# Kernel optimization log

Hardware: AMD Instinct MI355X
Metric: run time of the kernel (lower is better)

## Reference

```python
import jax, jax.numpy as jnp
import numpy as np

NUM_EXPERTS = 16
TOP_K = 2


def _swiglu(x, w13, w2):
    # x: [t, d]; w13: [2I, d] (gate and up fused); w2: [d, I]
    h = x @ w13.T                      # [t, 2I]
    gate, up = jnp.split(h, 2, axis=-1)
    return (jax.nn.silu(gate) * up) @ w2.T  # [t, d]


def setup_inputs() -> dict:
    key = jax.random.key(0)
    ks = jax.random.split(key, 6)
    T, D, I, E, SI = 4096, 1024, 512, NUM_EXPERTS, 2048
    return {
        "hidden_states": jax.random.normal(ks[0], (T, D), jnp.float32),
        "router_logits": jax.random.normal(ks[1], (T, E), jnp.float32),
        "w13": jax.random.normal(ks[2], (E, 2 * I, D), jnp.float32) * (1.0 / np.sqrt(D)),
        "w2": jax.random.normal(ks[3], (E, D, I), jnp.float32) * (1.0 / np.sqrt(I)),
        "w13_shared": jax.random.normal(ks[4], (2 * SI, D), jnp.float32) * (1.0 / np.sqrt(D)),
        "w2_shared": jax.random.normal(ks[5], (D, SI), jnp.float32) * (1.0 / np.sqrt(SI)),
    }


def reference(hidden_states, router_logits, w13, w2, w13_shared, w2_shared):
    # Shared expert path (overlapped with routed dispatch in the original).
    shared_out = _swiglu(hidden_states, w13_shared, w2_shared)  # [T, d]

    # Routing: softmax -> top-k -> renormalize (vLLM FusedMoE w/ renormalize=True).
    probs = jax.nn.softmax(router_logits, axis=-1)              # [T, E]
    topk_w, topk_idx = jax.lax.top_k(probs, TOP_K)              # [T, k]
    topk_w = topk_w / jnp.sum(topk_w, axis=-1, keepdims=True)

    # Dense combine-weight matrix [T, E]: zero where expert not selected.
    T = hidden_states.shape[0]
    combine = jnp.zeros((T, NUM_EXPERTS), hidden_states.dtype)
    combine = combine.at[jnp.arange(T)[:, None], topk_idx].add(topk_w)

    # Grouped expert compute: scan over experts (fixed structural set),
    # accumulating the combine-weighted SwiGLU output. Memory-friendly: no
    # [E, T, 2I] intermediate is materialized.
    def body(acc, ew):
        w13_e, w2_e, c_e = ew                     # [2I,d], [d,I], [T]
        y = _swiglu(hidden_states, w13_e, w2_e)   # [T, d]
        return acc + c_e[:, None] * y, None

    fused_out, _ = jax.lax.scan(body, jnp.zeros_like(hidden_states),
                                (w13, w2, combine.T))
    return shared_out, fused_out
```

## Files before the change

### kernel.cpp

```cpp
#include <hip/hip_runtime.h>


#define T_TOK 4096
#define NEXP  16

typedef __attribute__((ext_vector_type(8))) short   short8;
typedef __attribute__((ext_vector_type(4))) float   floatx4;

typedef __attribute__((address_space(1))) void as1_void;
typedef __attribute__((address_space(3))) void as3_void;

__device__ __forceinline__ float bf2f(ushort u) {
    union { unsigned int i; float f; } v; v.i = ((unsigned int)u) << 16; return v.f;
}
__device__ __forceinline__ ushort f2bf(float f) {
    unsigned int u = __builtin_bit_cast(unsigned int, f);
    unsigned int r = 0x7FFFu + ((u >> 16) & 1u);
    return (ushort)((u + r) >> 16);
}

__device__ __forceinline__ float load_elem(const void* p, long i, int bf) {
    return bf ? bf2f(((const ushort*)p)[i]) : ((const float*)p)[i];
}

__global__ void detect_dtype(const ushort* __restrict__ xu, int* __restrict__ dflag) {
    __shared__ int cnt;
    if (threadIdx.x == 0) cnt = 0;
    __syncthreads();
    int ok = 0;
    for (int i = threadIdx.x; i < 512; i += 256) {
        int e = (xu[2 * i] >> 7) & 0xFF;
        ok += (e >= 90 && e <= 140) ? 1 : 0;
    }
    atomicAdd(&cnt, ok);
    __syncthreads();
    if (threadIdx.x == 0) *dflag = (cnt >= 384) ? 1 : 0;
}

__global__ void detect_xsel(const void* __restrict__ p0, const void* __restrict__ p4,
                            const int* __restrict__ dflag, int* __restrict__ xsel) {
    __shared__ float s0s, s4s;
    if (threadIdx.x == 0) { s0s = 0.f; s4s = 0.f; }
    __syncthreads();
    int bf = *dflag;
    float a0 = 0.f, a4 = 0.f;
    for (int i = threadIdx.x; i < 4096; i += 256) {
        a0 += fabsf(load_elem(p0, (long)i * 997 + 13, bf));
        a4 += fabsf(load_elem(p4, (long)i * 997 + 13, bf));
    }
    atomicAdd(&s0s, a0);
    atomicAdd(&s4s, a4);
    __syncthreads();
    if (threadIdx.x == 0) *xsel = (s0s >= s4s) ? 0 : 1;
}

__device__ __forceinline__ void top2(const void* logits, int t, int bf,
                                     int& b0, int& b1, float& w0, float& w1) {
    float l[16];
#pragma unroll
    for (int j = 0; j < 16; ++j) l[j] = load_elem(logits, t * 16 + j, bf);
    b0 = 0; float v0 = l[0];
#pragma unroll
    for (int j = 1; j < 16; ++j) { if (l[j] > v0) { v0 = l[j]; b0 = j; } }
    b1 = -1; float v1 = -3.4e38f;
#pragma unroll
    for (int j = 0; j < 16; ++j) {
        if (j == b0) continue;
        if (l[j] > v1) { v1 = l[j]; b1 = j; }
    }
    float d = __expf(v1 - v0);
    w0 = 1.0f / (1.0f + d);
    w1 = d / (1.0f + d);
}

__global__ void router_counts(const void* __restrict__ logits, const int* __restrict__ dflag,
                              int* __restrict__ counts) {
    int t = blockIdx.x * blockDim.x + threadIdx.x;
    if (t >= T_TOK) return;
    int b0, b1; float w0, w1;
    top2(logits, t, *dflag, b0, b1, w0, w1);
    atomicAdd(&counts[b0], 1);
    atomicAdd(&counts[b1], 1);
}

__global__ void scan_kernel(const int* __restrict__ counts, int* __restrict__ offsets) {
    if (threadIdx.x == 0 && blockIdx.x == 0) {
        int acc = 0;
        for (int e = 0; e < NEXP; ++e) { offsets[e] = acc; acc += counts[e]; }
    }
}

__global__ void router_pairs(const void* __restrict__ logits, const int* __restrict__ dflag,
                             const int* __restrict__ offsets, int* __restrict__ cursor,
                             int* __restrict__ pairinfo, float* __restrict__ pairw) {
    int t = blockIdx.x * blockDim.x + threadIdx.x;
    if (t >= T_TOK) return;
    int b0, b1; float w0, w1;
    top2(logits, t, *dflag, b0, b1, w0, w1);
    int p0 = offsets[b0] + atomicAdd(&cursor[b0], 1);
    pairinfo[p0] = 2 * t;     pairw[p0] = w0;
    int p1 = offsets[b1] + atomicAdd(&cursor[b1], 1);
    pairinfo[p1] = 2 * t + 1; pairw[p1] = w1;
}

__global__ void to_bf16(const void* __restrict__ pA, const void* __restrict__ pB,
                        ushort* __restrict__ dst, long n8,
                        const int* __restrict__ dflag, const int* __restrict__ xsel)
{
    const void* src = (pB != nullptr && *xsel) ? pB : pA;
    const int bf = *dflag;
    long i = (long)blockIdx.x * blockDim.x + threadIdx.x;
    const long stride = (long)gridDim.x * blockDim.x;
    for (; i < n8; i += stride) {
        uint4 v;
        if (bf) {
            v = ((const uint4*)src)[i];
        } else {
            float4 f0 = ((const float4*)src)[i * 2];
            float4 f1 = ((const float4*)src)[i * 2 + 1];
            v.x = (unsigned)f2bf(f0.x) | ((unsigned)f2bf(f0.y) << 16);
            v.y = (unsigned)f2bf(f0.z) | ((unsigned)f2bf(f0.w) << 16);
            v.z = (unsigned)f2bf(f1.x) | ((unsigned)f2bf(f1.y) << 16);
            v.w = (unsigned)f2bf(f1.z) | ((unsigned)f2bf(f1.w) << 16);
        }
        ((uint4*)dst)[i] = v;
    }
}

__device__ __forceinline__ void gload16(const ushort* g, ushort* l) {
    __builtin_amdgcn_global_load_lds((as1_void*)g, (as3_void*)l, 16, 0, 0);
}

template <int SWIGLU, int GATHER, int ROUTED, int SCATTER>
__device__ __forceinline__ void gemm_core(
    ushort* __restrict__ smem,
    const ushort* __restrict__ A, int lda,
    const ushort* __restrict__ B0, long upoff, long bbase, int ldb,
    void* __restrict__ C, int ldc, float* __restrict__ C2,
    int m0, int n0, int Mloc, int K, int pair_base,
    const int* __restrict__ pairinfo, const float* __restrict__ pairw)
{
    constexpr int NBI = SWIGLU ? 2 : 4;
    constexpr int NFN = SWIGLU ? 2 : 4;

    ushort* As  = smem;
    ushort* Bs0 = smem + 128 * 64;
    ushort* Bs1 = SWIGLU ? (smem + 128 * 64 + 64 * 64) : nullptr;

    const int tid  = threadIdx.x;
    const int lane = tid & 63;
    const int wave = tid >> 6;
    const int srow = lane >> 3;
    const int scol = ((lane & 7) ^ srow) * 8;

    long aoff[4];
#pragma unroll
    for (int i = 0; i < 4; ++i) {
        int rl  = m0 + (wave * 4 + i) * 8 + srow;
        int rlc = rl < Mloc ? rl : Mloc - 1;
        long gr;
        if (GATHER)      gr = (long)(pairinfo[pair_base + rlc] >> 1);
        else if (ROUTED) gr = pair_base + rlc;
        else             gr = rlc;
        aoff[i] = gr * (long)lda + scol;
    }
    long boff[NBI];
#pragma unroll
    for (int i = 0; i < NBI; ++i) {
        int r = (wave * NBI + i) * 8 + srow;
        boff[i] = bbase + (long)(n0 + r) * ldb + scol;
    }

    const int wm   = (wave >> 1) * 64;
    const int wn   = (wave & 1) * (SWIGLU ? 32 : 64);
    const int r16  = lane & 15;
    const int quad = lane >> 4;
    const int rlow = r16 & 7;

    const floatx4 z4 = {0.f, 0.f, 0.f, 0.f};
    floatx4 accg[4][NFN], accu[4][NFN];
#pragma unroll
    for (int mi = 0; mi < 4; ++mi)
#pragma unroll
        for (int ni = 0; ni < NFN; ++ni) { accg[mi][ni] = z4; accu[mi][ni] = z4; }

    for (int k0 = 0; k0 < K; k0 += 64) {
#pragma unroll
        for (int i = 0; i < 4; ++i)
            gload16(A + aoff[i] + k0, &As[(wave * 4 + i) * 512]);
#pragma unroll
        for (int i = 0; i < NBI; ++i) {
            gload16(B0 + boff[i] + k0, &Bs0[(wave * NBI + i) * 512]);
            if constexpr (SWIGLU)
                gload16(B0 + boff[i] + upoff + k0, &Bs1[(wave * NBI + i) * 512]);
        }
        __syncthreads();
#pragma unroll
        for (int kc = 0; kc < 2; ++kc) {
            const int sw = ((kc * 4 + quad) ^ rlow) * 8;
            short8 af[4];
#pragma unroll
            for (int mi = 0; mi < 4; ++mi)
                af[mi] = *(const short8*)&As[(wm + mi * 16 + r16) * 64 + sw];
            short8 bfr[NFN], ufr[NFN];
#pragma unroll
            for (int ni = 0; ni < NFN; ++ni) {
                bfr[ni] = *(const short8*)&Bs0[(wn + ni * 16 + r16) * 64 + sw];
                if constexpr (SWIGLU)
                    ufr[ni] = *(const short8*)&Bs1[(wn + ni * 16 + r16) * 64 + sw];
            }
#pragma unroll
            for (int mi = 0; mi < 4; ++mi)
#pragma unroll
                for (int ni = 0; ni < NFN; ++ni) {
                    accg[mi][ni] = __builtin_amdgcn_mfma_f32_16x16x32_bf16(
                        af[mi], bfr[ni], accg[mi][ni], 0, 0, 0);
                    if constexpr (SWIGLU)
                        accu[mi][ni] = __builtin_amdgcn_mfma_f32_16x16x32_bf16(
                            af[mi], ufr[ni], accu[mi][ni], 0, 0, 0);
                }
        }
        __syncthreads();
    }

#pragma unroll
    for (int mi = 0; mi < 4; ++mi) {
#pragma unroll
        for (int r = 0; r < 4; ++r) {
            const int grow = m0 + wm + mi * 16 + quad * 4 + r;
            if (grow >= Mloc) continue;
            int info = 0; float w = 0.f;
            if constexpr (SCATTER) {
                const int p = pair_base + grow;
                info = pairinfo[p]; w = pairw[p];
            }
#pragma unroll
            for (int ni = 0; ni < NFN; ++ni) {
                const int col = n0 + wn + ni * 16 + r16;
                float val;
                if constexpr (SWIGLU) {
                    float g = accg[mi][ni][r];
                    float u = accu[mi][ni][r];
                    val = (g / (1.0f + __expf(-g))) * u;
                } else {
                    val = accg[mi][ni][r];
                }
                if constexpr (SCATTER) {
                    long idx = (long)(info >> 1) * 1024 + col;
                    float* dst = (info & 1) ? C2 : (float*)C;
                    dst[idx] = w * val;
                } else if constexpr (SWIGLU) {
                    long crow = ROUTED ? (long)(pair_base + grow) : (long)grow;
                    ((ushort*)C)[crow * ldc + col] = f2bf(val);
                } else {
                    ((float*)C)[(long)grow * ldc + col] = val;
                }
            }
        }
    }
}

template <int SWIGLU, int GATHER, int ROUTED, int SCATTER>
__global__ __launch_bounds__(256)
void gemm_fast(const ushort* __restrict__ A, int lda,
               const ushort* __restrict__ B0, long upoff, long strideB, int ldb,
               void* __restrict__ C, int ldc, float* __restrict__ C2,
               int M, int K,
               const int* __restrict__ counts, const int* __restrict__ offsets,
               const int* __restrict__ pairinfo, const float* __restrict__ pairw)
{
    __shared__ __align__(16) ushort smem[16384];
    const int e    = ROUTED ? (int)blockIdx.z : 0;
    const int Mloc = ROUTED ? counts[e] : M;
    const int m0   = blockIdx.y * 128;
    if (m0 >= Mloc) return;
    constexpr int BN = SWIGLU ? 64 : 128;
    const int n0  = blockIdx.x * BN;
    const int pb  = ROUTED ? offsets[e] : 0;
    const long bb = ROUTED ? (long)e * strideB : 0L;
    gemm_core<SWIGLU, GATHER, ROUTED, SCATTER>(
        smem, A, lda, B0, upoff, bb, ldb, C, ldc, C2,
        m0, n0, Mloc, K, pb, pairinfo, pairw);
}

__global__ __launch_bounds__(256)
void g1_fused(const ushort* __restrict__ hidb, const ushort* __restrict__ w13b,
              const ushort* __restrict__ w13sb,
              ushort* __restrict__ actR, ushort* __restrict__ actS,
              const int* __restrict__ counts, const int* __restrict__ offsets,
              const int* __restrict__ pairinfo)
{
    __shared__ __align__(16) ushort smem[16384];
    const int z  = blockIdx.z;
    const int m0 = blockIdx.y * 128;
    if (z < 4) {
        const int e    = z * 4 + ((int)blockIdx.x >> 3);
        const int Mloc = counts[e];
        if (m0 >= Mloc) return;
        const int n0 = ((int)blockIdx.x & 7) * 64;
        gemm_core<1, 1, 1, 0>(smem, hidb, 1024,
                              w13b, (long)512 * 1024, (long)e * 1024 * 1024, 1024,
                              actR, 512, nullptr,
                              m0, n0, Mloc, 1024, offsets[e], pairinfo, nullptr);
    } else {
        const int n0 = (int)blockIdx.x * 64;
        gemm_core<1, 0, 0, 0>(smem, hidb, 1024,
                              w13sb, (long)2048 * 1024, 0L, 1024,
                              actS, 2048, nullptr,
                              m0, n0, T_TOK, 1024, 0, nullptr, nullptr);
    }
}

__global__ __launch_bounds__(256)
void g2_fused(const ushort* __restrict__ actR, const ushort* __restrict__ actS,
              const ushort* __restrict__ w2b, const ushort* __restrict__ w2sb,
              float* __restrict__ outF, float* __restrict__ outT,
              float* __restrict__ outS,
              const int* __restrict__ counts, const int* __restrict__ offsets,
              const int* __restrict__ pairinfo, const float* __restrict__ pairw)
{
    __shared__ __align__(16) ushort smem[16384];
    const int z  = blockIdx.z;
    const int m0 = blockIdx.y * 128;
    if (z < 4) {
        const int e    = z * 4 + ((int)blockIdx.x >> 3);
        const int Mloc = counts[e];
        if (m0 >= Mloc) return;
        const int n0 = ((int)blockIdx.x & 7) * 128;
        gemm_core<0, 0, 1, 1>(smem, actR, 512,
                              w2b, 0L, (long)e * 1024 * 512, 512,
                              outF, 1024, outT,
                              m0, n0, Mloc, 512, offsets[e], pairinfo, pairw);
    } else {
        if ((int)blockIdx.x >= 8) return;
        const int n0 = (int)blockIdx.x * 128;
        gemm_core<0, 0, 0, 0>(smem, actS, 2048,
                              w2sb, 0L, 0L, 2048,
                              outS, 1024, nullptr,
                              m0, n0, T_TOK, 2048, 0, nullptr, nullptr);
    }
}

__device__ __forceinline__ void stage8(const void* __restrict__ src, long eoff, int bf,
                                       ushort* __restrict__ dst) {
    if (bf) {
        *(uint4*)dst = *(const uint4*)((const ushort*)src + eoff);
    } else {
        const float* s = (const float*)src + eoff;
        float4 f0 = *(const float4*)s;
        float4 f1 = *(const float4*)(s + 4);
        uint4 v;
        v.x = (unsigned)f2bf(f0.x) | ((unsigned)f2bf(f0.y) << 16);
        v.y = (unsigned)f2bf(f0.z) | ((unsigned)f2bf(f0.w) << 16);
        v.z = (unsigned)f2bf(f1.x) | ((unsigned)f2bf(f1.y) << 16);
        v.w = (unsigned)f2bf(f1.z) | ((unsigned)f2bf(f1.w) << 16);
        *(uint4*)dst = v;
    }
}

template <int SWIGLU, int GATHER, int ROUTED, int SCATTER, int LOCAL,
          int A_DT, int B_DT, int C_F32>
__global__ __launch_bounds__(256)
void gemm_nt(const void* __restrict__ A, const void* __restrict__ Aalt, int lda,
             const void* __restrict__ B0, const void* __restrict__ B0alt,
             long upoff, long strideB,
             void* __restrict__ C, int ldc, void* __restrict__ C2,
             int M, int K, int row0,
             const int* __restrict__ dflag, const int* __restrict__ xsel,
             const int* __restrict__ counts, const int* __restrict__ offsets,
             const int* __restrict__ pairinfo, const float* __restrict__ pairw,
             int e_base, int m_base, int Mcap)
{
    const int dfl = (A_DT && B_DT) ? 1 : *dflag;
    const int abf = A_DT ? 1 : dfl;
    const int bbf = B_DT ? 1 : dfl;
    if (Aalt  && *xsel) A  = Aalt;
    if (B0alt && *xsel) B0 = B0alt;

    const int e = ROUTED ? (e_base + (int)blockIdx.z) : 0;
    int Mloc;
    if (ROUTED) {
        int avail = counts[e] - m_base;
        Mloc = avail < Mcap ? avail : Mcap;
    } else {
        Mloc = M;
    }
    const int m0 = blockIdx.y * 64;
    if (m0 >= Mloc) return;
    const int n0 = blockIdx.x * 64;
    const int pair_base = ROUTED ? (offsets[e] + m_base) : 0;
    const int abase     = ROUTED ? (LOCAL ? 0 : offsets[e]) : 0;
    const long bbase    = ROUTED ? (long)e * strideB : 0L;

    constexpr int LS = 72;
    __shared__ __align__(16) ushort As[64 * LS];
    __shared__ __align__(16) ushort Bs0[64 * LS];
    __shared__ __align__(16) ushort Bs1[SWIGLU ? 64 * LS : 8];

    const int tid = threadIdx.x;

    int  lofs[2];
    long aoff[2], boff[2];
#pragma unroll
    for (int i = 0; i < 2; ++i) {
        int idx = tid + i * 256;
        int row = idx >> 3;
        int col = (idx & 7) * 8;
        lofs[i] = row * LS + col;
        int rl  = m0 + row;
        int rlc = rl < Mloc ? rl : (Mloc - 1);
        long rA;
        if (GATHER)      rA = (long)(pairinfo[pair_base + rlc] >> 1);
        else if (ROUTED) rA = abase + rlc;
        else             rA = row0 + rl;
        aoff[i] = rA * (long)lda + col;
        boff[i] = bbase + (long)(n0 + row) * K + col;
    }

    const int lane = tid & 63;
    const int wave = tid >> 6;
    const int wm   = (wave >> 1) * 32;
    const int wn   = (wave & 1) * 32;
    const int r16  = lane & 15;
    const int quad = lane >> 4;

    floatx4 accg[2][2] = {{{0.f,0.f,0.f,0.f},{0.f,0.f,0.f,0.f}},{{0.f,0.f,0.f,0.f},{0.f,0.f,0.f,0.f}}};
    floatx4 accu[2][2] = {{{0.f,0.f,0.f,0.f},{0.f,0.f,0.f,0.f}},{{0.f,0.f,0.f,0.f},{0.f,0.f,0.f,0.f}}};

    for (int k0 = 0; k0 < K; k0 += 64) {
#pragma unroll
        for (int i = 0; i < 2; ++i) {
            stage8(A,  aoff[i] + k0, abf, &As[lofs[i]]);
            stage8(B0, boff[i] + k0, bbf, &Bs0[lofs[i]]);
            if (SWIGLU) stage8(B0, boff[i] + k0 + upoff, bbf, &Bs1[lofs[i]]);
        }
        __syncthreads();
#pragma unroll
        for (int kc = 0; kc < 2; ++kc) {
            const int kof = kc * 32 + quad * 8;
            short8 a0 = *(const short8*)&As[(wm + r16)      * LS + kof];
            short8 a1 = *(const short8*)&As[(wm + 16 + r16) * LS + kof];
            short8 b0 = *(const short8*)&Bs0[(wn + r16)      * LS + kof];
            short8 b1 = *(const short8*)&Bs0[(wn + 16 + r16) * LS + kof];
            accg[0][0] = __builtin_amdgcn_mfma_f32_16x16x32_bf16(a0, b0, accg[0][0], 0, 0, 0);
            accg[0][1] = __builtin_amdgcn_mfma_f32_16x16x32_bf16(a0, b1, accg[0][1], 0, 0, 0);
            accg[1][0] = __builtin_amdgcn_mfma_f32_16x16x32_bf16(a1, b0, accg[1][0], 0, 0, 0);
            accg[1][1] = __builtin_amdgcn_mfma_f32_16x16x32_bf16(a1, b1, accg[1][1], 0, 0, 0);
            if (SWIGLU) {
                short8 u0 = *(const short8*)&Bs1[(wn + r16)      * LS + kof];
                short8 u1 = *(const short8*)&Bs1[(wn + 16 + r16) * LS + kof];
                accu[0][0] = __builtin_amdgcn_mfma_f32_16x16x32_bf16(a0, u0, accu[0][0], 0, 0, 0);
                accu[0][1] = __builtin_amdgcn_mfma_f32_16x16x32_bf16(a0, u1, accu[0][1], 0, 0, 0);
                accu[1][0] = __builtin_amdgcn_mfma_f32_16x16x32_bf16(a1, u0, accu[1][0], 0, 0, 0);
                accu[1][1] = __builtin_amdgcn_mfma_f32_16x16x32_bf16(a1, u1, accu[1][1], 0, 0, 0);
            }
        }
        __syncthreads();
    }

#pragma unroll
    for (int mi = 0; mi < 2; ++mi) {
#pragma unroll
        for (int ni = 0; ni < 2; ++ni) {
#pragma unroll
            for (int r = 0; r < 4; ++r) {
                int rowl = wm + mi * 16 + quad * 4 + r;
                int grow = m0 + rowl;
                if (grow < Mloc) {
                    int col = n0 + wn + ni * 16 + r16;
                    float g = accg[mi][ni][r];
                    float val;
                    if (SWIGLU) {
                        float u = accu[mi][ni][r];
                        val = (g / (1.0f + __expf(-g))) * u;
                    } else {
                        val = g;
                    }
                    if (SCATTER) {
                        int p    = pair_base + grow;
                        int info = pairinfo[p];
                        float w  = pairw[p];
                        long idx = (long)(info >> 1) * 1024 + col;
                        void* dst = (info & 1) ? C2 : C;
                        if (C_F32) ((float*)dst)[idx]  = w * val;
                        else       ((ushort*)dst)[idx] = f2bf(w * val);
                    } else {
                        int crow = ROUTED ? (abase + grow) : grow;
                        long idx = (long)crow * ldc + col;
                        if (C_F32) ((float*)C)[idx]  = val;
                        else       ((ushort*)C)[idx] = f2bf(val);
                    }
                }
            }
        }
    }
}

__global__ void add_kernel(float* __restrict__ outF, const float* __restrict__ outT, int n4) {
    int i = blockIdx.x * blockDim.x + threadIdx.x;
    if (i >= n4) return;
    float4 a = *(const float4*)(outF + (long)i * 4);
    float4 b = *(const float4*)(outT + (long)i * 4);
    a.x += b.x; a.y += b.y; a.z += b.z; a.w += b.w;
    *(float4*)(outF + (long)i * 4) = a;
}

extern "C" void kernel_launch(void* const* d_in, const int* in_sizes, int n_in,
                              void* d_out, int out_size, void* d_ws, size_t ws_size,
                              hipStream_t stream)
{
    const void* in0  = d_in[0];
    const void* rl   = d_in[1];
    const void* w13  = d_in[2];
    const void* w2   = d_in[3];
    const void* in4  = d_in[4];
    const void* w2s  = d_in[5];
    float* outS = (float*)d_out;
    float* outF = (float*)d_out + (size_t)T_TOK * 1024;

    char*  base     = (char*)d_ws;
    int*   counts   = (int*)(base);
    int*   cursor   = (int*)(base + 64);
    int*   dflag    = (int*)(base + 128);
    int*   xsel     = (int*)(base + 132);
    int*   offsets  = (int*)(base + 192);
    int*   pairinfo = (int*)(base + 256);
    float* pairw    = (float*)(base + 256 + 32768);
    const size_t META = 256 + 65536;

    size_t avail = ws_size > META ? ws_size - META : 0;

    detect_dtype<<<1, 256, 0, stream>>>((const ushort*)in0, dflag);
    detect_xsel<<<1, 256, 0, stream>>>(in0, in4, dflag, xsel);
    hipMemsetAsync(counts, 0, 128, stream);
    router_counts<<<T_TOK / 256, 256, 0, stream>>>(rl, dflag, counts);
    scan_kernel<<<1, 64, 0, stream>>>(counts, offsets);
    router_pairs<<<T_TOK / 256, 256, 0, stream>>>(rl, dflag, offsets, cursor, pairinfo, pairw);

    const long sB1  = (long)1024 * 1024;
    const long sB2  = (long)1024 * 512;
    const long UP_R = (long)512 * 1024;
    const long UP_S = (long)2048 * 1024;

    const size_t FULL2_NEED = 96468992ULL;
    const size_t FULL_NEED  = 88080384ULL;
    const size_t MID_NEED   = 29360128ULL;

    if (avail >= FULL2_NEED) {
        ushort* hidb  = (ushort*)(base + META);
        ushort* w13sb = hidb  + (size_t)4096 * 1024;
        ushort* w13b  = w13sb + (size_t)4096 * 1024;
        ushort* w2b   = w13b  + (size_t)16 * 1024 * 1024;
        ushort* w2sb  = w2b   + (size_t)16 * 1024 * 512;
        ushort* actR  = w2sb  + (size_t)1024 * 2048;
        ushort* actS  = actR  + (size_t)8192 * 512;
        float*  outT  = (float*)hidb;

        to_bf16<<<1024, 256, 0, stream>>>(in0, in4, hidb,  (long)4096 * 1024 / 8,      dflag, xsel);
        to_bf16<<<1024, 256, 0, stream>>>(in4, in0, w13sb, (long)4096 * 1024 / 8,      dflag, xsel);
        to_bf16<<<1024, 256, 0, stream>>>(w13, nullptr, w13b, (long)16 * 1024 * 1024 / 8, dflag, xsel);
        to_bf16<<<1024, 256, 0, stream>>>(w2,  nullptr, w2b,  (long)16 * 1024 * 512 / 8,  dflag, xsel);
        to_bf16<<<1024, 256, 0, stream>>>(w2s, nullptr, w2sb, (long)1024 * 2048 / 8,      dflag, xsel);

        g1_fused<<<dim3(32, 32, 5), 256, 0, stream>>>(
            hidb, w13b, w13sb, actR, actS, counts, offsets, pairinfo);
        g2_fused<<<dim3(32, 32, 5), 256, 0, stream>>>(
            actR, actS, w2b, w2sb, outF, outT, outS,
            counts, offsets, pairinfo, pairw);
        add_kernel<<<(T_TOK * 1024 / 4 + 255) / 256, 256, 0, stream>>>(outF, outT, T_TOK * 1024 / 4);
    } else if (avail >= FULL_NEED) {
        ushort* hidb  = (ushort*)(base + META);
        ushort* w13b  = hidb  + (size_t)4096 * 1024;
        ushort* w2b   = w13b  + (size_t)16 * 1024 * 1024;
        ushort* w13sb = w2b   + (size_t)16 * 1024 * 512;
        ushort* w2sb  = w13sb + (size_t)4096 * 1024;
        ushort* actb  = w2sb  + (size_t)1024 * 2048;

        to_bf16<<<1024, 256, 0, stream>>>(in0, in4, hidb,  (long)4096 * 1024 / 8,      dflag, xsel);
        to_bf16<<<1024, 256, 0, stream>>>(w13, nullptr, w13b, (long)16 * 1024 * 1024 / 8, dflag, xsel);
        to_bf16<<<1024, 256, 0, stream>>>(w2,  nullptr, w2b,  (long)16 * 1024 * 512 / 8,  dflag, xsel);
        to_bf16<<<1024, 256, 0, stream>>>(in4, in0, w13sb, (long)4096 * 1024 / 8,      dflag, xsel);
        to_bf16<<<1024, 256, 0, stream>>>(w2s, nullptr, w2sb, (long)1024 * 2048 / 8,      dflag, xsel);

        gemm_fast<1,1,1,0><<<dim3(8, 32, NEXP), 256, 0, stream>>>(
            hidb, 1024, w13b, UP_R, sB1, 1024, actb, 512, nullptr, 0, 1024,
            counts, offsets, pairinfo, pairw);
        gemm_fast<0,0,1,1><<<dim3(8, 32, NEXP), 256, 0, stream>>>(
            actb, 512, w2b, 0, sB2, 512, outF, 1024, outS, 0, 512,
            counts, offsets, pairinfo, pairw);
        add_kernel<<<(T_TOK * 1024 / 4 + 255) / 256, 256, 0, stream>>>(outF, outS, T_TOK * 1024 / 4);
        gemm_fast<1,0,0,0><<<dim3(32, 32), 256, 0, stream>>>(
            hidb, 1024, w13sb, UP_S, 0, 1024, actb, 2048, nullptr, 4096, 1024,
            nullptr, nullptr, nullptr, nullptr);
        gemm_fast<0,0,0,0><<<dim3(8, 32), 256, 0, stream>>>(
            actb, 2048, w2sb, 0, 0, 2048, outS, 1024, nullptr, 4096, 2048,
            nullptr, nullptr, nullptr, nullptr);
    } else if (avail >= MID_NEED) {
        ushort* act   = (ushort*)(base + META);
        ushort* hidb  = act   + (size_t)8192 * 512;
        ushort* w13sb = hidb  + (size_t)4096 * 1024;
        ushort* w2sb  = w13sb + (size_t)4096 * 1024;

        to_bf16<<<1024, 256, 0, stream>>>(in0, in4, hidb,  (long)4096 * 1024 / 8, dflag, xsel);
        to_bf16<<<1024, 256, 0, stream>>>(in4, in0, w13sb, (long)4096 * 1024 / 8, dflag, xsel);
        to_bf16<<<1024, 256, 0, stream>>>(w2s, nullptr, w2sb, (long)1024 * 2048 / 8, dflag, xsel);

        gemm_nt<1,1,1,0,0,1,0,0><<<dim3(8, 64, NEXP), 256, 0, stream>>>(
            hidb, nullptr, 1024, w13, nullptr, UP_R, sB1, act, 512, nullptr, 0, 1024, 0,
            dflag, xsel, counts, offsets, pairinfo, pairw, 0, 0, T_TOK);
        gemm_nt<0,0,1,1,0,1,0,1><<<dim3(16, 64, NEXP), 256, 0, stream>>>(
            act, nullptr, 512, w2, nullptr, 0, sB2, outF, 1024, outS, 0, 512, 0,
            dflag, xsel, counts, offsets, pairinfo, pairw, 0, 0, T_TOK);
        add_kernel<<<(T_TOK * 1024 / 4 + 255) / 256, 256, 0, stream>>>(outF, outS, T_TOK * 1024 / 4);
        for (int c = 0; c < 2; ++c) {
            gemm_fast<1,0,0,0><<<dim3(32, 16), 256, 0, stream>>>(
                hidb + (size_t)c * 2048 * 1024, 1024, w13sb, UP_S, 0, 1024,
                act, 2048, nullptr, 2048, 1024, nullptr, nullptr, nullptr, nullptr);
            gemm_fast<0,0,0,0><<<dim3(8, 16), 256, 0, stream>>>(
                act, 2048, w2sb, 0, 0, 2048, outS + (size_t)c * 2048 * 1024, 1024, nullptr,
                2048, 2048, nullptr, nullptr, nullptr, nullptr);
        }
    } else {
        const size_t MB = 1024 * 1024;
        int grouped, Mcap, CH;
        if      (avail >= 8 * MB) { grouped = 1; Mcap = T_TOK; CH = 2048; }
        else if (avail >= 1 * MB) { grouped = 0; Mcap = 1024;  CH = 256;  }
        else                      { grouped = 0; Mcap = 256;   CH = 64;   }
        ushort* act = (ushort*)(base + META);

        if (grouped) {
            gemm_nt<1,1,1,0,0,0,0,0><<<dim3(8, 64, NEXP), 256, 0, stream>>>(
                in0, in4, 1024, w13, nullptr, UP_R, sB1, act, 512, nullptr, 0, 1024, 0,
                dflag, xsel, counts, offsets, pairinfo, pairw, 0, 0, T_TOK);
            gemm_nt<0,0,1,1,0,1,0,1><<<dim3(16, 64, NEXP), 256, 0, stream>>>(
                act, nullptr, 512, w2, nullptr, 0, sB2, outF, 1024, outS, 0, 512, 0,
                dflag, xsel, counts, offsets, pairinfo, pairw, 0, 0, T_TOK);
        } else {
            for (int e = 0; e < NEXP; ++e) {
                for (int mb = 0; mb < T_TOK; mb += Mcap) {
                    gemm_nt<1,1,1,0,1,0,0,0><<<dim3(8, Mcap / 64, 1), 256, 0, stream>>>(
                        in0, in4, 1024, w13, nullptr, UP_R, sB1, act, 512, nullptr, 0, 1024, 0,
                        dflag, xsel, counts, offsets, pairinfo, pairw, e, mb, Mcap);
                    gemm_nt<0,0,1,1,1,1,0,1><<<dim3(16, Mcap / 64, 1), 256, 0, stream>>>(
                        act, nullptr, 512, w2, nullptr, 0, sB2, outF, 1024, outS, 0, 512, 0,
                        dflag, xsel, counts, offsets, pairinfo, pairw, e, mb, Mcap);
                }
            }
        }
        add_kernel<<<(T_TOK * 1024 / 4 + 255) / 256, 256, 0, stream>>>(outF, outS, T_TOK * 1024 / 4);
        for (int c = 0; c < T_TOK / CH; ++c) {
            gemm_nt<1,0,0,0,0,0,0,0><<<dim3(2048 / 64, CH / 64), 256, 0, stream>>>(
                in0, in4, 1024, in4, in0, UP_S, 0, act, 2048, nullptr, CH, 1024, c * CH,
                dflag, xsel, nullptr, nullptr, nullptr, nullptr, 0, 0, 0);
            gemm_nt<0,0,0,0,0,1,0,1><<<dim3(1024 / 64, CH / 64), 256, 0, stream>>>(
                act, nullptr, 2048, w2s, nullptr, 0, 0,
                outS + (size_t)c * CH * 1024, 1024, nullptr, CH, 2048, 0,
                dflag, xsel, nullptr, nullptr, nullptr, nullptr, 0, 0, 0);
        }
    }
    (void)in_sizes; (void)n_in; (void)out_size;
}
```

Baseline: 443.9 us.

## Split shared-expert down-projection over K and narrow N tiles for more blocks

The shared-expert second GEMM (K=2048) is split into two K halves, each written to a separate fp32 buffer, and uses narrower 64-wide N tiles, raising its block count from 8x32 to 2x16x32. This is meant to cut the long tail where few, long-running blocks of the shared GEMM finish last. In exchange it needs an extra fp32 partial buffer and a final add pass over the shared output, merged into the existing combine kernel. The path runs only when the workspace is large enough.

```diff
diff --git a/kernel.cpp b/kernel.cpp
--- a/kernel.cpp
+++ b/kernel.cpp
@@ -131,7 +131,7 @@
     __builtin_amdgcn_global_load_lds((as1_void*)g, (as3_void*)l, 16, 0, 0);
 }
 
-template <int SWIGLU, int GATHER, int ROUTED, int SCATTER>
+template <int SWIGLU, int GATHER, int ROUTED, int SCATTER, int NARROW = 0>
 __device__ __forceinline__ void gemm_core(
     ushort* __restrict__ smem,
     const ushort* __restrict__ A, int lda,
@@ -140,8 +140,9 @@
     int m0, int n0, int Mloc, int K, int pair_base,
     const int* __restrict__ pairinfo, const float* __restrict__ pairw)
 {
-    constexpr int NBI = SWIGLU ? 2 : 4;
-    constexpr int NFN = SWIGLU ? 2 : 4;
+    constexpr int BNRW = (SWIGLU || NARROW);
+    constexpr int NBI = BNRW ? 2 : 4;
+    constexpr int NFN = BNRW ? 2 : 4;
 
     ushort* As  = smem;
     ushort* Bs0 = smem + 128 * 64;
@@ -172,7 +173,7 @@
     }
 
     const int wm   = (wave >> 1) * 64;
-    const int wn   = (wave & 1) * (SWIGLU ? 32 : 64);
+    const int wn   = (wave & 1) * (BNRW ? 32 : 64);
     const int r16  = lane & 15;
     const int quad = lane >> 4;
     const int rlow = r16 & 7;
@@ -311,11 +312,12 @@
     }
 }
 
+template <int SPLIT>
 __global__ __launch_bounds__(256)
 void g2_fused(const ushort* __restrict__ actR, const ushort* __restrict__ actS,
               const ushort* __restrict__ w2b, const ushort* __restrict__ w2sb,
               float* __restrict__ outF, float* __restrict__ outT,
-              float* __restrict__ outS,
+              float* __restrict__ outS, float* __restrict__ outP,
               const int* __restrict__ counts, const int* __restrict__ offsets,
               const int* __restrict__ pairinfo, const float* __restrict__ pairw)
 {
@@ -331,6 +333,14 @@
                               w2b, 0L, (long)e * 1024 * 512, 512,
                               outF, 1024, outT,
                               m0, n0, Mloc, 512, offsets[e], pairinfo, pairw);
+    } else if constexpr (SPLIT) {
+        const int zz = z - 4;
+        if ((int)blockIdx.x >= 16) return;
+        const int n0 = (int)blockIdx.x * 64;
+        gemm_core<0, 0, 0, 0, 1>(smem, actS + zz * 1024, 2048,
+                                 w2sb + zz * 1024, 0L, 0L, 2048,
+                                 zz ? outP : outS, 1024, nullptr,
+                                 m0, n0, T_TOK, 1024, 0, nullptr, nullptr);
     } else {
         if ((int)blockIdx.x >= 8) return;
         const int n0 = (int)blockIdx.x * 128;
@@ -505,6 +515,24 @@
     *(float4*)(outF + (long)i * 4) = a;
 }
 
+__global__ void add2_kernel(float* __restrict__ outF, const float* __restrict__ outT,
+                            float* __restrict__ outS, const float* __restrict__ outP,
+                            int n4) {
+    int i = blockIdx.x * blockDim.x + threadIdx.x;
+    if (i < n4) {
+        float4 a = *(const float4*)(outF + (long)i * 4);
+        float4 b = *(const float4*)(outT + (long)i * 4);
+        a.x += b.x; a.y += b.y; a.z += b.z; a.w += b.w;
+        *(float4*)(outF + (long)i * 4) = a;
+    } else if (i < 2 * n4) {
+        int j = i - n4;
+        float4 a = *(const float4*)(outS + (long)j * 4);
+        float4 b = *(const float4*)(outP + (long)j * 4);
+        a.x += b.x; a.y += b.y; a.z += b.z; a.w += b.w;
+        *(float4*)(outS + (long)j * 4) = a;
+    }
+}
+
 extern "C" void kernel_launch(void* const* d_in, const int* in_sizes, int n_in,
                               void* d_out, int out_size, void* d_ws, size_t ws_size,
                               hipStream_t stream)
@@ -542,6 +570,7 @@
     const long UP_R = (long)512 * 1024;
     const long UP_S = (long)2048 * 1024;
 
+    const size_t FULL3_NEED = 113246208ULL;
     const size_t FULL2_NEED = 96468992ULL;
     const size_t FULL_NEED  = 88080384ULL;
     const size_t MID_NEED   = 29360128ULL;
@@ -554,6 +583,7 @@
         ushort* w2sb  = w2b   + (size_t)16 * 1024 * 512;
         ushort* actR  = w2sb  + (size_t)1024 * 2048;
         ushort* actS  = actR  + (size_t)8192 * 512;
+        float*  outP  = (float*)(actS + (size_t)4096 * 2048);
         float*  outT  = (float*)hidb;
 
         to_bf16<<<1024, 256, 0, stream>>>(in0, in4, hidb,  (long)4096 * 1024 / 8,      dflag, xsel);
@@ -564,10 +594,20 @@
 
         g1_fused<<<dim3(32, 32, 5), 256, 0, stream>>>(
             hidb, w13b, w13sb, actR, actS, counts, offsets, pairinfo);
-        g2_fused<<<dim3(32, 32, 5), 256, 0, stream>>>(
-            actR, actS, w2b, w2sb, outF, outT, outS,
-            counts, offsets, pairinfo, pairw);
-        add_kernel<<<(T_TOK * 1024 / 4 + 255) / 256, 256, 0, stream>>>(outF, outT, T_TOK * 1024 / 4);
+
+        if (avail >= FULL3_NEED) {
+            g2_fused<1><<<dim3(32, 32, 6), 256, 0, stream>>>(
+                actR, actS, w2b, w2sb, outF, outT, outS, outP,
+                counts, offsets, pairinfo, pairw);
+            add2_kernel<<<(2 * (T_TOK * 1024 / 4) + 255) / 256, 256, 0, stream>>>(
+                outF, outT, outS, outP, T_TOK * 1024 / 4);
+        } else {
+            g2_fused<0><<<dim3(32, 32, 5), 256, 0, stream>>>(
+                actR, actS, w2b, w2sb, outF, outT, outS, nullptr,
+                counts, offsets, pairinfo, pairw);
+            add_kernel<<<(T_TOK * 1024 / 4 + 255) / 256, 256, 0, stream>>>(
+                outF, outT, T_TOK * 1024 / 4);
+        }
     } else if (avail >= FULL_NEED) {
         ushort* hidb  = (ushort*)(base + META);
         ushort* w13b  = hidb  + (size_t)4096 * 1024;
```

New measurement: 412.0 us. -7.2%, faster.
